# Performance work log

Measured on AMD Instinct MI355X. Metric: run time of the kernel, lower is better.

The kernel has to match this reference:

```python
import jax, jax.numpy as jnp
import numpy as np

E4M3 = jnp.float8_e4m3fn  # forward fp8 dtype (HYBRID recipe fwd)

def fp8_qdq(x, fp8_dtype):
    # quantize (scale=1) to fp8 then dequantize back: models precision loss
    return x.astype(fp8_dtype).astype(x.dtype)

def setup_inputs() -> dict:
    key = jax.random.key(0)
    k1, k2 = jax.random.split(key)
    tokens, d_in, units = 4096, 1024, 4096
    x = jax.random.normal(k1, (tokens, d_in), dtype=jnp.float32)
    # kernel_initializer default: RandomNormal(mean=0.0, stddev=0.023)
    kernel = jax.random.normal(k2, (d_in, units), dtype=jnp.float32) * 0.023
    bias = jnp.zeros((units,), dtype=jnp.float32)
    return {"x": x, "kernel": kernel, "bias": bias}

def reference(x, kernel, bias):
    # fp8 quantize/dequantize prologue on activations and weights
    xq = fp8_qdq(x, E4M3)          # [tokens, d_in]
    kq = fp8_qdq(kernel, E4M3)     # [d_in, units]
    out = jnp.matmul(xq, kq) + bias  # [tokens, units]
    # gelu approximate=True (tanh approximation)
    return jax.nn.gelu(out, approximate=True)
```

## Files before the change

### kernel.cpp

```cpp
#include <hip/hip_runtime.h>
#include <hip/hip_bf16.h>

typedef float f32x4 __attribute__((ext_vector_type(4)));
typedef long  l2    __attribute__((ext_vector_type(2)));

__device__ __forceinline__ void gld16(const void* g, void* l) {
    __builtin_amdgcn_global_load_lds(
        (const __attribute__((address_space(1))) void*)g,
        (__attribute__((address_space(3))) void*)l,
        16, 0, 0);
}

__device__ __forceinline__ float gelu_tanh(float x) {
    float u = 0.7978845608028654f * x * (1.0f + 0.044715f * x * x);
    float e = __expf(2.0f * u);
    float t = 1.0f - 2.0f / (e + 1.0f);
    return 0.5f * x * (1.0f + t);
}


__global__ __launch_bounds__(256) void quantA_kernel(
        const float* __restrict__ in, unsigned char* __restrict__ out,
        int n4, int K) {
    int i = blockIdx.x * 256 + threadIdx.x;
    if (i >= n4) return;
    float4 v = reinterpret_cast<const float4*>(in)[i];
    int pk = 0;
    pk = __builtin_amdgcn_cvt_pk_fp8_f32(v.x, v.y, pk, false);
    pk = __builtin_amdgcn_cvt_pk_fp8_f32(v.z, v.w, pk, true);
    const long k4 = (long)i * 4;
    const int  row = (int)(k4 / K);
    const int  k   = (int)(k4 % K);
    const int  o   = k & 63;
    const int  g   = (o & 31) >> 3;
    const int  s   = (o & 7) + ((o >> 5) & 1) * 8;
    const int  c   = g ^ ((row >> 1) & 3);
    *reinterpret_cast<unsigned int*>(
        out + (long)row * K + (k & ~63) + (c << 4) + s) = (unsigned int)pk;
}

__global__ __launch_bounds__(256) void quantBT_kernel(
        const float* __restrict__ B, unsigned char* __restrict__ BT,
        int K, int N) {
    __shared__ unsigned char lds[64 * 68];
    const int tid = threadIdx.x;
    const int n0 = blockIdx.x * 64;
    const int k0 = blockIdx.y * 64;

    #pragma unroll
    for (int p = 0; p < 4; ++p) {
        int s = p * 256 + tid;
        int r = s >> 4;
        int c = s & 15;
        float4 v = *reinterpret_cast<const float4*>(
            B + (long)(k0 + r) * N + n0 + c * 4);
        int pk = 0;
        pk = __builtin_amdgcn_cvt_pk_fp8_f32(v.x, v.y, pk, false);
        pk = __builtin_amdgcn_cvt_pk_fp8_f32(v.z, v.w, pk, true);
        *reinterpret_cast<unsigned int*>(&lds[r * 68 + c * 4]) = (unsigned int)pk;
    }
    __syncthreads();
    #pragma unroll
    for (int p = 0; p < 4; ++p) {
        int sidx = p * 256 + tid;
        int n  = sidx >> 4;
        int kg = sidx & 15;
        unsigned int w = 0;
        #pragma unroll
        for (int j = 0; j < 4; ++j)
            w |= (unsigned int)lds[(kg * 4 + j) * 68 + n] << (8 * j);
        const int nn = n0 + n;
        const int o  = kg * 4;
        const int g  = (o & 31) >> 3;
        const int s  = (o & 7) + ((o >> 5) & 1) * 8;
        const int c  = g ^ ((nn >> 1) & 3);
        *reinterpret_cast<unsigned int*>(
            BT + (long)nn * K + k0 + (c << 4) + s) = w;
    }
}

__global__ __launch_bounds__(512, 2) void gemm_fp8_kernel(
        const unsigned char* __restrict__ A,
        const unsigned char* __restrict__ BT,
        const float* __restrict__ bias,
        float* __restrict__ out,
        int M, int N, int K) {
    constexpr int BM = 256, BN = 256, BK = 64;
    __shared__ unsigned char lds[3][2][BM * BK];

    const int tid  = threadIdx.x;
    const int lane = tid & 63;
    const int wid  = tid >> 6;
    const int wm   = wid >> 2;
    const int wn   = wid & 3;

    const int bid = blockIdx.x;
    const int xcd = bid & 7, idx = bid >> 3;
    const int tile_m = (xcd & 3) * 4 + (idx & 3);
    const int tile_n = (xcd >> 2) * 8 + (idx >> 2);
    const int m0 = tile_m * BM, n0 = tile_n * BN;

    const int lrow = lane & 15;
    const int kgrp = lane >> 4;
    const int chunkoff = ((kgrp ^ ((lrow >> 1) & 3)) << 4);

    const int srow   = tid >> 2;
    const int schunk = (tid & 3) << 4;
    const unsigned char* gA = A  + (long)(m0 + srow) * K + schunk;
    const unsigned char* gB = BT + (long)(n0 + srow) * K + schunk;
    const int ldst = wid * 1024;

    const int aBase = (wm * 128 + lrow) * 64 + chunkoff;
    const int bBase = (wn * 64  + lrow) * 64 + chunkoff;

    f32x4 acc[8][4] = {};

    const int NT = K / BK;

#define STAGE(BB, OP, H, TT)                                              \
    gld16((OP ? gB : gA) + (long)(H) * 128 * K + (long)(TT) * BK,         \
          &lds[BB][OP][(H) * 8192 + ldst])

#define PHASE_HEAD()                                                      \
    __builtin_amdgcn_sched_barrier(0);                                    \
    __builtin_amdgcn_s_barrier();                                         \
    asm volatile("s_waitcnt lgkmcnt(0)" ::: "memory");                    \
    __builtin_amdgcn_sched_barrier(0);                                    \
    __builtin_amdgcn_s_setprio(1)

#define PHASE_TAIL()                                                      \
    __builtin_amdgcn_s_setprio(0);                                        \
    __builtin_amdgcn_sched_barrier(0);                                    \
    __builtin_amdgcn_s_barrier()

#define MFMA_Q(AI0, BJ0, BREG)                                            \
    _Pragma("unroll") for (int ks = 0; ks < 2; ++ks)                      \
    _Pragma("unroll") for (int fi = 0; fi < 4; ++fi)                      \
    _Pragma("unroll") for (int fj = 0; fj < 2; ++fj)                      \
        acc[(AI0) + fi][(BJ0) + fj] =                                     \
            __builtin_amdgcn_mfma_f32_16x16x32_fp8_fp8(                   \
                a[fi][ks], BREG[fj][ks], acc[(AI0) + fi][(BJ0) + fj], 0, 0, 0)

    STAGE(0, 0, 0, 0); STAGE(0, 0, 1, 0); STAGE(0, 1, 0, 0); STAGE(0, 1, 1, 0);
    STAGE(1, 0, 0, 1); STAGE(1, 0, 1, 1); STAGE(1, 1, 0, 1); STAGE(1, 1, 1, 1);
    asm volatile("s_waitcnt vmcnt(4)" ::: "memory");
    __builtin_amdgcn_sched_barrier(0);
    __builtin_amdgcn_s_barrier();

    int b = 0, b2 = 2;
    for (int t = 0; t < NT; ++t) {
        const unsigned char* sAb = &lds[b][0][0];
        const unsigned char* sBb = &lds[b][1][0];
        const bool st = (t + 2 < NT);
        l2 a[4], br0[2], br1[2];

        #pragma unroll
        for (int f = 0; f < 4; ++f)
            a[f] = *reinterpret_cast<const l2*>(sAb + aBase + f * 1024);
        #pragma unroll
        for (int f = 0; f < 2; ++f)
            br0[f] = *reinterpret_cast<const l2*>(sBb + bBase + f * 1024);
        if (st) { STAGE(b2, 0, 0, t + 2); }
        PHASE_HEAD();
        MFMA_Q(0, 0, br0);
        PHASE_TAIL();

        #pragma unroll
        for (int f = 0; f < 2; ++f)
            br1[f] = *reinterpret_cast<const l2*>(sBb + bBase + 2048 + f * 1024);
        if (st) { STAGE(b2, 0, 1, t + 2); }
        PHASE_HEAD();
        MFMA_Q(0, 2, br1);
        PHASE_TAIL();

        #pragma unroll
        for (int f = 0; f < 4; ++f)
            a[f] = *reinterpret_cast<const l2*>(sAb + aBase + 4096 + f * 1024);
        if (st) { STAGE(b2, 1, 0, t + 2); }
        PHASE_HEAD();
        MFMA_Q(4, 0, br0);
        PHASE_TAIL();

        if (st) { STAGE(b2, 1, 1, t + 2); }
        __builtin_amdgcn_sched_barrier(0);
        __builtin_amdgcn_s_barrier();
        __builtin_amdgcn_s_setprio(1);
        MFMA_Q(4, 2, br1);
        __builtin_amdgcn_s_setprio(0);
        __builtin_amdgcn_sched_barrier(0);
        if (t < NT - 1) {
            if (st) { asm volatile("s_waitcnt vmcnt(4)" ::: "memory"); }
            else    { asm volatile("s_waitcnt vmcnt(0)" ::: "memory"); }
            __builtin_amdgcn_sched_barrier(0);
            __builtin_amdgcn_s_barrier();
        }
        b  = (b  == 2) ? 0 : b  + 1;
        b2 = (b2 == 2) ? 0 : b2 + 1;
    }

    #pragma unroll
    for (int bj = 0; bj < 4; ++bj) {
        const int col = n0 + wn * 64 + bj * 16 + lrow;
        const float bv = bias[col];
        #pragma unroll
        for (int ai = 0; ai < 8; ++ai) {
            const int rbase = m0 + wm * 128 + ai * 16 + kgrp * 4;
            f32x4 v = acc[ai][bj];
            #pragma unroll
            for (int r = 0; r < 4; ++r) {
                float xv = v[r] + bv;
                out[(long)(rbase + r) * N + col] = gelu_tanh(xv);
            }
        }
    }
#undef STAGE
#undef PHASE_HEAD
#undef PHASE_TAIL
#undef MFMA_Q
}

extern "C" void kernel_launch(void* const* d_in, const int* in_sizes, int n_in,
                              void* d_out, int out_size, void* d_ws, size_t ws_size,
                              hipStream_t stream) {
    const float* x    = (const float*)d_in[0];
    const float* w    = (const float*)d_in[1];
    const float* bias = (const float*)d_in[2];
    float* out = (float*)d_out;

    const int units  = in_sizes[2];
    const int dmodel = in_sizes[1] / units;
    const int tokens = in_sizes[0] / dmodel;

    unsigned char* Aq  = (unsigned char*)d_ws;
    unsigned char* BTq = Aq + (size_t)tokens * dmodel;

    const int n4a = tokens * dmodel / 4;
    quantA_kernel<<<dim3(n4a / 256), dim3(256), 0, stream>>>(
        x, Aq, n4a, dmodel);

    quantBT_kernel<<<dim3(units / 64, dmodel / 64), dim3(256), 0, stream>>>(
        w, BTq, dmodel, units);

    const int nblocks = (tokens / 256) * (units / 256);
    gemm_fp8_kernel<<<dim3(nblocks), dim3(512), 0, stream>>>(
        Aq, BTq, bias, out, tokens, units, dmodel);
}
```

Baseline: 56.18 us.

## Shrink GEMM tile to 128x256, raise occupancy, stage epilogue through LDS

Halves the M tile to 128 and merges the A and B LDS buffers into one triple-buffered array. This doubles the block count to 512 and lowers per-thread accumulator registers so launch bounds can ask for 4 blocks per CU, and it remaps tiles across XCDs. The epilogue now writes GELU results to LDS and reads them back as 16-byte vectorised row stores instead of scattered scalar column stores. Each loaded B tile is reused over fewer rows, so operand reuse drops and global load traffic per FLOP goes up.

```diff
diff --git a/kernel.cpp b/kernel.cpp
--- a/kernel.cpp
+++ b/kernel.cpp
@@ -79,14 +79,14 @@
     }
 }
 
-__global__ __launch_bounds__(512, 2) void gemm_fp8_kernel(
+__global__ __launch_bounds__(512, 4) void gemm_fp8_kernel(
         const unsigned char* __restrict__ A,
         const unsigned char* __restrict__ BT,
         const float* __restrict__ bias,
         float* __restrict__ out,
         int M, int N, int K) {
-    constexpr int BM = 256, BN = 256, BK = 64;
-    __shared__ unsigned char lds[3][2][BM * BK];
+    constexpr int BM = 128, BN = 256, BK = 64;
+    __shared__ unsigned char lds[3][(BM + BN) * BK];
 
     const int tid  = threadIdx.x;
     const int lane = tid & 63;
@@ -96,8 +96,8 @@
 
     const int bid = blockIdx.x;
     const int xcd = bid & 7, idx = bid >> 3;
-    const int tile_m = (xcd & 3) * 4 + (idx & 3);
-    const int tile_n = (xcd >> 2) * 8 + (idx >> 2);
+    const int tile_m = (xcd >> 1) * 8 + (idx & 7);
+    const int tile_n = (xcd & 1) * 8 + (idx >> 3);
     const int m0 = tile_m * BM, n0 = tile_n * BN;
 
     const int lrow = lane & 15;
@@ -108,18 +108,19 @@
     const int schunk = (tid & 3) << 4;
     const unsigned char* gA = A  + (long)(m0 + srow) * K + schunk;
     const unsigned char* gB = BT + (long)(n0 + srow) * K + schunk;
-    const int ldst = wid * 1024;
-
-    const int aBase = (wm * 128 + lrow) * 64 + chunkoff;
-    const int bBase = (wn * 64  + lrow) * 64 + chunkoff;
-
-    f32x4 acc[8][4] = {};
+
+    const int aBase = (wm * 64 + lrow) * 64 + chunkoff;
+    const int bBase = 8192 + (wn * 64 + lrow) * 64 + chunkoff;
+
+    f32x4 acc[4][4] = {};
 
     const int NT = K / BK;
 
-#define STAGE(BB, OP, H, TT)                                              \
-    gld16((OP ? gB : gA) + (long)(H) * 128 * K + (long)(TT) * BK,         \
-          &lds[BB][OP][(H) * 8192 + ldst])
+#define STAGE_A(BB, TT)                                                   \
+    gld16(gA + (long)(TT) * BK, &lds[BB][wid * 1024])
+#define STAGE_B(BB, H, TT)                                                \
+    gld16(gB + (long)(H) * 128 * K + (long)(TT) * BK,                     \
+          &lds[BB][8192 + (H) * 8192 + wid * 1024])
 
 #define PHASE_HEAD()                                                      \
     __builtin_amdgcn_sched_barrier(0);                                    \
@@ -133,63 +134,59 @@
     __builtin_amdgcn_sched_barrier(0);                                    \
     __builtin_amdgcn_s_barrier()
 
-#define MFMA_Q(AI0, BJ0, BREG)                                            \
+#define MFMA_Q(AI0, BJ0, AR, BR)                                          \
     _Pragma("unroll") for (int ks = 0; ks < 2; ++ks)                      \
-    _Pragma("unroll") for (int fi = 0; fi < 4; ++fi)                      \
+    _Pragma("unroll") for (int fi = 0; fi < 2; ++fi)                      \
     _Pragma("unroll") for (int fj = 0; fj < 2; ++fj)                      \
         acc[(AI0) + fi][(BJ0) + fj] =                                     \
             __builtin_amdgcn_mfma_f32_16x16x32_fp8_fp8(                   \
-                a[fi][ks], BREG[fj][ks], acc[(AI0) + fi][(BJ0) + fj], 0, 0, 0)
-
-    STAGE(0, 0, 0, 0); STAGE(0, 0, 1, 0); STAGE(0, 1, 0, 0); STAGE(0, 1, 1, 0);
-    STAGE(1, 0, 0, 1); STAGE(1, 0, 1, 1); STAGE(1, 1, 0, 1); STAGE(1, 1, 1, 1);
-    asm volatile("s_waitcnt vmcnt(4)" ::: "memory");
+                AR[fi][ks], BR[fj][ks], acc[(AI0) + fi][(BJ0) + fj], 0, 0, 0)
+
+    STAGE_A(0, 0); STAGE_B(0, 0, 0); STAGE_B(0, 1, 0);
+    STAGE_A(1, 1); STAGE_B(1, 0, 1); STAGE_B(1, 1, 1);
+    asm volatile("s_waitcnt vmcnt(3)" ::: "memory");
     __builtin_amdgcn_sched_barrier(0);
     __builtin_amdgcn_s_barrier();
 
     int b = 0, b2 = 2;
     for (int t = 0; t < NT; ++t) {
-        const unsigned char* sAb = &lds[b][0][0];
-        const unsigned char* sBb = &lds[b][1][0];
+        const unsigned char* sL = &lds[b][0];
         const bool st = (t + 2 < NT);
-        l2 a[4], br0[2], br1[2];
-
-        #pragma unroll
-        for (int f = 0; f < 4; ++f)
-            a[f] = *reinterpret_cast<const l2*>(sAb + aBase + f * 1024);
+        l2 a01[2], a23[2], b01[2], b23[2];
+
+        #pragma unroll
+        for (int f = 0; f < 2; ++f) {
+            a01[f] = *reinterpret_cast<const l2*>(sL + aBase + f * 1024);
+            b01[f] = *reinterpret_cast<const l2*>(sL + bBase + f * 1024);
+        }
+        if (st) { STAGE_A(b2, t + 2); }
+        PHASE_HEAD();
+        MFMA_Q(0, 0, a01, b01);
+        PHASE_TAIL();
+
         #pragma unroll
         for (int f = 0; f < 2; ++f)
-            br0[f] = *reinterpret_cast<const l2*>(sBb + bBase + f * 1024);
-        if (st) { STAGE(b2, 0, 0, t + 2); }
+            b23[f] = *reinterpret_cast<const l2*>(sL + bBase + 2048 + f * 1024);
+        if (st) { STAGE_B(b2, 0, t + 2); }
         PHASE_HEAD();
-        MFMA_Q(0, 0, br0);
+        MFMA_Q(0, 2, a01, b23);
         PHASE_TAIL();
 
         #pragma unroll
         for (int f = 0; f < 2; ++f)
-            br1[f] = *reinterpret_cast<const l2*>(sBb + bBase + 2048 + f * 1024);
-        if (st) { STAGE(b2, 0, 1, t + 2); }
+            a23[f] = *reinterpret_cast<const l2*>(sL + aBase + 2048 + f * 1024);
+        if (st) { STAGE_B(b2, 1, t + 2); }
         PHASE_HEAD();
-        MFMA_Q(0, 2, br1);
+        MFMA_Q(2, 0, a23, b01);
         PHASE_TAIL();
 
-        #pragma unroll
-        for (int f = 0; f < 4; ++f)
-            a[f] = *reinterpret_cast<const l2*>(sAb + aBase + 4096 + f * 1024);
-        if (st) { STAGE(b2, 1, 0, t + 2); }
-        PHASE_HEAD();
-        MFMA_Q(4, 0, br0);
-        PHASE_TAIL();
-
-        if (st) { STAGE(b2, 1, 1, t + 2); }
-        __builtin_amdgcn_sched_barrier(0);
         __builtin_amdgcn_s_barrier();
         __builtin_amdgcn_s_setprio(1);
-        MFMA_Q(4, 2, br1);
+        MFMA_Q(2, 2, a23, b23);
         __builtin_amdgcn_s_setprio(0);
         __builtin_amdgcn_sched_barrier(0);
         if (t < NT - 1) {
-            if (st) { asm volatile("s_waitcnt vmcnt(4)" ::: "memory"); }
+            if (st) { asm volatile("s_waitcnt vmcnt(3)" ::: "memory"); }
             else    { asm volatile("s_waitcnt vmcnt(0)" ::: "memory"); }
             __builtin_amdgcn_sched_barrier(0);
             __builtin_amdgcn_s_barrier();
@@ -198,22 +195,34 @@
         b2 = (b2 == 2) ? 0 : b2 + 1;
     }
 
-    #pragma unroll
-    for (int bj = 0; bj < 4; ++bj) {
-        const int col = n0 + wn * 64 + bj * 16 + lrow;
-        const float bv = bias[col];
-        #pragma unroll
-        for (int ai = 0; ai < 8; ++ai) {
-            const int rbase = m0 + wm * 128 + ai * 16 + kgrp * 4;
-            f32x4 v = acc[ai][bj];
+    __syncthreads();
+    float* eplds = reinterpret_cast<float*>(&lds[0][0]) + wid * 1088;
+    const int  col0   = n0 + wn * 64;
+    const long rbase0 = m0 + wm * 64;
+    float bv[4];
+    #pragma unroll
+    for (int bj = 0; bj < 4; ++bj) bv[bj] = bias[col0 + bj * 16 + lrow];
+
+    #pragma unroll
+    for (int ai = 0; ai < 4; ++ai) {
+        #pragma unroll
+        for (int bj = 0; bj < 4; ++bj) {
             #pragma unroll
             for (int r = 0; r < 4; ++r) {
-                float xv = v[r] + bv;
-                out[(long)(rbase + r) * N + col] = gelu_tanh(xv);
+                float xv = acc[ai][bj][r] + bv[bj];
+                eplds[(kgrp * 4 + r) * 68 + bj * 16 + lrow] = gelu_tanh(xv);
             }
         }
-    }
-#undef STAGE
+        #pragma unroll
+        for (int s = 0; s < 4; ++s) {
+            f32x4 v = *reinterpret_cast<const f32x4*>(
+                eplds + (s * 4 + kgrp) * 68 + lrow * 4);
+            *reinterpret_cast<f32x4*>(
+                out + (rbase0 + ai * 16 + s * 4 + kgrp) * N + col0 + lrow * 4) = v;
+        }
+    }
+#undef STAGE_A
+#undef STAGE_B
 #undef PHASE_HEAD
 #undef PHASE_TAIL
 #undef MFMA_Q
@@ -241,7 +250,7 @@
     quantBT_kernel<<<dim3(units / 64, dmodel / 64), dim3(256), 0, stream>>>(
         w, BTq, dmodel, units);
 
-    const int nblocks = (tokens / 256) * (units / 256);
+    const int nblocks = (tokens / 128) * (units / 256);
     gemm_fp8_kernel<<<dim3(nblocks), dim3(512), 0, stream>>>(
         Aq, BTq, bias, out, tokens, units, dmodel);
 }
```

New measurement: 49.09 us. -12.6%, faster.
